# Kernel tuning notes

Hardware: AMD Instinct MI355X
Metric: run time of the kernel (lower is better)

Reference implementation:

```python
import jax, jax.numpy as jnp
import numpy as np

B, L, D = 16, 2048, 256

def setup_inputs() -> dict:
    key = jax.random.key(0)
    k1, k2 = jax.random.split(key)
    inp = jax.random.normal(k1, (B, L, D), dtype=jnp.float32)
    # Linear(2*dim, 1, bias=False) weight, torch layout [out=1, in=2*dim]
    v_w = jax.random.normal(k2, (1, 2 * D), dtype=jnp.float32) * (1.0 / np.sqrt(2 * D))
    return {"inp": inp, "v_w": v_w}


def reference(inp, v_w):
    # score[b,i,j] = cat(query=inp[b,i], key=inp[b,j]) . v_w
    # decomposes exactly into two rank-1 projections broadcast-summed.
    dim = inp.shape[-1]
    wq = v_w[0, :dim]   # multiplies the query half (unsqueeze(1) -> index i)
    wk = v_w[0, dim:]   # multiplies the key half (unsqueeze(2) -> index j)
    sq = jnp.einsum('bld,d->bl', inp, wq)          # [B,L]
    sk = jnp.einsum('bld,d->bl', inp, wk)          # [B,L]
    score = sq[:, :, None] + sk[:, None, :]        # [B,L,L]
    attn = jax.nn.softmax(score, axis=2)           # Softmax(2)
    out = jnp.einsum('bij,bjd->bid', attn, inp)    # bmm
    return (out, attn)
```

## Files before the change

kernel.cpp:

```cpp
#include <hip/hip_runtime.h>

#define BB 16
#define LL 2048
#define DD 256
#define D1B 2048
#define OUTB 256
#define ATTB 2048

typedef float vf4 __attribute__((ext_vector_type(4)));

__global__ void __launch_bounds__(256)
d1_pass(const float* __restrict__ inp, const float* __restrict__ wk,
        float* __restrict__ e, float* __restrict__ upart, float* __restrict__ zpart) {
    const int t = threadIdx.x, lane = t & 63, wid = t >> 6;
    const int blk = blockIdx.x;
    const int row0 = blk * 16 + wid * 4;

    const float4 w = *reinterpret_cast<const float4*>(wk + lane * 4);
    float4 acc = make_float4(0.f, 0.f, 0.f, 0.f);
    float zsum = 0.f;

    #pragma unroll
    for (int r = 0; r < 4; ++r) {
        const int row = row0 + r;
        const float4 a = *reinterpret_cast<const float4*>(inp + (size_t)row * DD + lane * 4);
        float dot = a.x * w.x + a.y * w.y + a.z * w.z + a.w * w.w;
        #pragma unroll
        for (int off = 32; off >= 1; off >>= 1) dot += __shfl_xor(dot, off, 64);
        const float ev = __expf(dot);
        if (lane == 0) e[row] = ev;
        zsum += ev;
        acc.x = fmaf(ev, a.x, acc.x);
        acc.y = fmaf(ev, a.y, acc.y);
        acc.z = fmaf(ev, a.z, acc.z);
        acc.w = fmaf(ev, a.w, acc.w);
    }

    __shared__ float uacc[4][DD];
    __shared__ float zw[4];
    *reinterpret_cast<float4*>(&uacc[wid][lane * 4]) = acc;
    if (lane == 0) zw[wid] = zsum;
    __syncthreads();
    upart[(size_t)blk * DD + t] = uacc[0][t] + uacc[1][t] + uacc[2][t] + uacc[3][t];
    if (t == 0) zpart[blk] = zw[0] + zw[1] + zw[2] + zw[3];
}

__global__ void __launch_bounds__(256)
d2_write(const float* __restrict__ upart, const float* __restrict__ zpart,
         const float* __restrict__ e, float* __restrict__ out) {
    const int blk = blockIdx.x, t = threadIdx.x;
    const int lane = t & 63, wid = t >> 6;
    __shared__ float sInv;
    __shared__ float ov[DD];

    const bool isOut = blk < OUTB;
    const int b = isOut ? (blk >> 4) : ((blk - OUTB) >> 7);

    if (wid == 0) {
        const float2 z2 = *reinterpret_cast<const float2*>(zpart + b * 128 + lane * 2);
        float z = z2.x + z2.y;
        #pragma unroll
        for (int off = 32; off >= 1; off >>= 1) z += __shfl_xor(z, off, 64);
        if (lane == 0) sInv = 1.0f / z;
    }
    __syncthreads();
    const float iz = sInv;
    vf4* dst = (vf4*)out;

    if (isOut) {
        const float* up = upart + ((size_t)b * 128) * DD + t;
        float acc = 0.f;
        #pragma unroll 8
        for (int k = 0; k < 128; ++k) acc += up[(size_t)k * DD];
        ov[t] = acc * iz;
        __syncthreads();
        const vf4 o = ((const vf4*)ov)[t & 63];
        size_t obase = (size_t)b * 131072 + (size_t)(blk & 15) * 8192 + t;
        #pragma unroll 4
        for (int it = 0; it < 32; ++it)
            __builtin_nontemporal_store(o, &dst[obase + (size_t)it * 256]);
    } else {
        const int s = (blk - OUTB) & 127;
        const vf4* e4 = (const vf4*)e;
        const vf4 ev0 = e4[(b << 9) + t] * iz;
        const vf4 ev1 = e4[(b << 9) + 256 + t] * iz;
        size_t abase = (size_t)2097152 + (size_t)b * 1048576 + (size_t)s * 8192 + t;
        #pragma unroll 4
        for (int it = 0; it < 32; it += 2) {
            __builtin_nontemporal_store(ev0, &dst[abase + (size_t)it * 256]);
            __builtin_nontemporal_store(ev1, &dst[abase + (size_t)it * 256 + 256]);
        }
    }
}

extern "C" void kernel_launch(void* const* d_in, const int* in_sizes, int n_in,
                              void* d_out, int out_size, void* d_ws, size_t ws_size,
                              hipStream_t stream) {
    const float* inp = (const float*)d_in[0];
    const float* vw  = (const float*)d_in[1];
    float* out = (float*)d_out;
    float* ws  = (float*)d_ws;

    float* e     = ws;
    float* upart = ws + 32768;
    float* zpart = ws + 557056;

    d1_pass <<<D1B, 256, 0, stream>>>(inp, vw + DD, e, upart, zpart);
    d2_write<<<OUTB + ATTB, 256, 0, stream>>>(upart, zpart, e, out);
}
```

Before: 67.76 us.

## Split partial reduction into finalize kernel and balance write kernel blocks

The upart/zpart reduction moves out of the write kernel into a small 16-block finalize kernel that produces the normalized output vector and 1/Z per batch. The write kernel then becomes uniform: every block writes 4 output rows and 8 attention row groups, so work is evenly balanced. Before, 256 blocks each did a 128-step reduction and the Z reduction was redundantly recomputed in all 2304 blocks. The cost is an extra kernel launch and a serialized, low-parallelism 16-block stage.

```diff
diff --git a/kernel.cpp b/kernel.cpp
--- a/kernel.cpp
+++ b/kernel.cpp
@@ -4,8 +4,6 @@
 #define LL 2048
 #define DD 256
 #define D1B 2048
-#define OUTB 256
-#define ATTB 2048
 
 typedef float vf4 __attribute__((ext_vector_type(4)));
 
@@ -46,16 +44,11 @@
 }
 
 __global__ void __launch_bounds__(256)
-d2_write(const float* __restrict__ upart, const float* __restrict__ zpart,
-         const float* __restrict__ e, float* __restrict__ out) {
-    const int blk = blockIdx.x, t = threadIdx.x;
+d15_finalize(const float* __restrict__ upart, const float* __restrict__ zpart,
+             float* __restrict__ outv, float* __restrict__ Zinv) {
+    const int b = blockIdx.x, t = threadIdx.x;
     const int lane = t & 63, wid = t >> 6;
     __shared__ float sInv;
-    __shared__ float ov[DD];
-
-    const bool isOut = blk < OUTB;
-    const int b = isOut ? (blk >> 4) : ((blk - OUTB) >> 7);
-
     if (wid == 0) {
         const float2 z2 = *reinterpret_cast<const float2*>(zpart + b * 128 + lane * 2);
         float z = z2.x + z2.y;
@@ -63,33 +56,37 @@
         for (int off = 32; off >= 1; off >>= 1) z += __shfl_xor(z, off, 64);
         if (lane == 0) sInv = 1.0f / z;
     }
+    const float* up = upart + ((size_t)b * 128) * DD + t;
+    float acc = 0.f;
+    #pragma unroll 8
+    for (int k = 0; k < 128; ++k) acc += up[(size_t)k * DD];
     __syncthreads();
-    const float iz = sInv;
+    outv[b * DD + t] = acc * sInv;
+    if (t == 0) Zinv[b] = sInv;
+}
+
+__global__ void __launch_bounds__(256)
+d2_write(const float* __restrict__ outv, const float* __restrict__ Zinv,
+         const float* __restrict__ e, float* __restrict__ out) {
+    const int blk = blockIdx.x, t = threadIdx.x;
+    const int b = blk >> 7, k = blk & 127;
+    const float iz = Zinv[b];
+    const vf4* e4 = (const vf4*)e;
+    const vf4 ev0 = e4[(b << 9) + t] * iz;
+    const vf4 ev1 = e4[(b << 9) + 256 + t] * iz;
+    const vf4 ov  = ((const vf4*)outv)[(b << 6) + (t & 63)];
     vf4* dst = (vf4*)out;
 
-    if (isOut) {
-        const float* up = upart + ((size_t)b * 128) * DD + t;
-        float acc = 0.f;
-        #pragma unroll 8
-        for (int k = 0; k < 128; ++k) acc += up[(size_t)k * DD];
-        ov[t] = acc * iz;
-        __syncthreads();
-        const vf4 o = ((const vf4*)ov)[t & 63];
-        size_t obase = (size_t)b * 131072 + (size_t)(blk & 15) * 8192 + t;
-        #pragma unroll 4
-        for (int it = 0; it < 32; ++it)
-            __builtin_nontemporal_store(o, &dst[obase + (size_t)it * 256]);
-    } else {
-        const int s = (blk - OUTB) & 127;
-        const vf4* e4 = (const vf4*)e;
-        const vf4 ev0 = e4[(b << 9) + t] * iz;
-        const vf4 ev1 = e4[(b << 9) + 256 + t] * iz;
-        size_t abase = (size_t)2097152 + (size_t)b * 1048576 + (size_t)s * 8192 + t;
-        #pragma unroll 4
-        for (int it = 0; it < 32; it += 2) {
-            __builtin_nontemporal_store(ev0, &dst[abase + (size_t)it * 256]);
-            __builtin_nontemporal_store(ev1, &dst[abase + (size_t)it * 256 + 256]);
-        }
+    size_t obase = (size_t)b * 131072 + (size_t)k * 1024 + t;
+    #pragma unroll
+    for (int it = 0; it < 4; ++it)
+        __builtin_nontemporal_store(ov, &dst[obase + (size_t)it * 256]);
+
+    size_t abase = (size_t)2097152 + (size_t)b * 1048576 + (size_t)k * 8192 + t;
+    #pragma unroll 4
+    for (int it = 0; it < 32; it += 2) {
+        __builtin_nontemporal_store(ev0, &dst[abase + (size_t)it * 256]);
+        __builtin_nontemporal_store(ev1, &dst[abase + (size_t)it * 256 + 256]);
     }
 }
 
@@ -104,7 +101,10 @@
     float* e     = ws;
     float* upart = ws + 32768;
     float* zpart = ws + 557056;
+    float* outv  = ws + 559104;
+    float* Zinv  = ws + 563200;
 
-    d1_pass <<<D1B, 256, 0, stream>>>(inp, vw + DD, e, upart, zpart);
-    d2_write<<<OUTB + ATTB, 256, 0, stream>>>(upart, zpart, e, out);
+    d1_pass     <<<D1B, 256, 0, stream>>>(inp, vw + DD, e, upart, zpart);
+    d15_finalize<<<BB,  256, 0, stream>>>(upart, zpart, outv, Zinv);
+    d2_write    <<<2048, 256, 0, stream>>>(outv, Zinv, e, out);
 }
```

Measured after the change: 75.28 us. +11.1%, slower.
